# Performance work log

Measured on AMD Instinct MI355X. Metric: run time of the kernel, lower is better.

The kernel has to match this reference:

```python
import jax, jax.numpy as jnp
import numpy as np

B, N, F, FE, H, C = 2, 2048, 128, 8, 4, 64
LEAKY_ALPHA = 0.2
NEG_INF = -1e9


def setup_inputs() -> dict:
    key = jax.random.key(0)
    ks = jax.random.split(key, 8)
    return {
        "X": jax.random.normal(ks[0], (B, N, F), jnp.float32),
        "A": jax.random.uniform(ks[1], (B, N, N), jnp.float32),
        "E": jax.random.normal(ks[2], (B, N, N, FE), jnp.float32),
        "W_edge": jax.random.normal(ks[3], (FE, 1), jnp.float32) * 0.1,
        "b_edge": jnp.zeros((1,), jnp.float32),
        "W_gat": jax.random.normal(ks[4], (H, F, C), jnp.float32) * 0.05,
        "a_src": jax.random.normal(ks[5], (H, C), jnp.float32) * 0.1,
        "a_dst": jax.random.normal(ks[6], (H, C), jnp.float32) * 0.1,
        "b_gat": jnp.zeros((H * C,), jnp.float32),
        "ln_gamma": jnp.ones((H * C,), jnp.float32),
        "ln_beta": jnp.zeros((H * C,), jnp.float32),
    }


def reference(X, A, E, W_edge, b_edge, W_gat, a_src, a_dst, b_gat, ln_gamma, ln_beta):
    # --- edge gate: sigmoid(Dense_1(E)) -> [B,N,N], multiply into adjacency ---
    edge_w = jax.nn.sigmoid(jnp.einsum("bije,eo->bijo", E, W_edge) + b_edge)
    A = A * edge_w[..., 0]  # [B,N,N]

    # --- multi-head dense GAT (spektral GATConv, concat_heads, elu) ---
    h = jnp.einsum("bnf,hfc->bnhc", X, W_gat)  # [B,N,H,C]
    s_src = jnp.einsum("bnhc,hc->bnh", h, a_src)  # [B,N,H]
    s_dst = jnp.einsum("bnhc,hc->bnh", h, a_dst)
    # e_ij = LeakyReLU(src_i + dst_j): [B,N(i),N(j),H]
    logits = jax.nn.leaky_relu(s_src[:, :, None, :] + s_dst[:, None, :, :],
                               negative_slope=LEAKY_ALPHA)
    mask = jnp.where(A == 0.0, NEG_INF, 0.0)[..., None]  # [B,N,N,1]
    attn = jax.nn.softmax(logits + mask, axis=2)  # softmax over neighbors j
    out = jnp.einsum("bijh,bjhc->bihc", attn, h)  # [B,N,H,C]
    out = out.reshape(B, N, H * C) + b_gat
    out = jax.nn.elu(out)

    # --- LayerNorm over the feature axis (inference: dropout is identity) ---
    mu = jnp.mean(out, axis=-1, keepdims=True)
    var = jnp.var(out, axis=-1, keepdims=True)
    out = (out - mu) * jax.lax.rsqrt(var + 1e-3) * ln_gamma + ln_beta
    return out
```

## Files before the change

kernel.cpp:

```cpp
#include <hip/hip_runtime.h>
#include <hip/hip_bf16.h>


#define BB 2
#define NN 2048
#define FF 128
#define HH 4
#define CC 64
#define HC 256
#define TN 8
#define JB (NN / 8)
#define LOG2E 1.4426950408889634f

typedef __attribute__((ext_vector_type(8))) short short8;
typedef __attribute__((ext_vector_type(4))) float f32x4;

__device__ __forceinline__ float wave_sum(float v) {
#pragma unroll
    for (int m = 32; m >= 1; m >>= 1) v += __shfl_xor(v, m, 64);
    return v;
}

__device__ __forceinline__ unsigned short bf16rne(float x) {
    unsigned u = __float_as_uint(x);
    return (unsigned short)((u + 0x7fffu + ((u >> 16) & 1u)) >> 16);
}

__global__ __launch_bounds__(256) void k1_proj(
    const float* __restrict__ X, const float* __restrict__ Adj,
    const float* __restrict__ Wg,
    const float* __restrict__ a_src, const float* __restrict__ a_dst,
    unsigned short* __restrict__ hT, float* __restrict__ ssT,
    float* __restrict__ sdT, unsigned char* __restrict__ zT)
{
    const int blk = blockIdx.x;
    const int b  = blk / (NN / TN);
    const int n0 = (blk % (NN / TN)) * TN;
    const int tid = threadIdx.x;
    const int h = tid >> 6, c = tid & 63;

    float hv[TN];
#pragma unroll
    for (int r = 0; r < TN; ++r) hv[r] = 0.f;

    const float* xp = X + (size_t)(b * NN + n0) * FF;

#pragma unroll 4
    for (int f4 = 0; f4 < FF / 4; ++f4) {
        const int f = f4 * 4;
        const float w0 = Wg[(h * FF + f + 0) * CC + c];
        const float w1 = Wg[(h * FF + f + 1) * CC + c];
        const float w2 = Wg[(h * FF + f + 2) * CC + c];
        const float w3 = Wg[(h * FF + f + 3) * CC + c];
#pragma unroll
        for (int r = 0; r < TN; ++r) {
            float4 x4 = *(const float4*)(xp + r * FF + f);
            hv[r] = fmaf(x4.x, w0, hv[r]);
            hv[r] = fmaf(x4.y, w1, hv[r]);
            hv[r] = fmaf(x4.z, w2, hv[r]);
            hv[r] = fmaf(x4.w, w3, hv[r]);
        }
    }

    union { short8 v; unsigned short u[8]; } pk;
#pragma unroll
    for (int r = 0; r < TN; ++r) pk.u[r] = bf16rne(hv[r]);
    *(short8*)&hT[((((size_t)b * HH + h) * JB + (n0 >> 3)) * CC + c) * 8] = pk.v;

    const float as = a_src[tid];
    const float ad = a_dst[tid];
#pragma unroll
    for (int r = 0; r < TN; ++r) {
        const int n = n0 + r;
        float s1 = wave_sum(hv[r] * as);
        float s2 = wave_sum(hv[r] * ad);
        if (c == 0) {
            ssT[(b * HH + h) * NN + n] = s1 * LOG2E;
            sdT[(b * HH + h) * NN + n] = s2 * LOG2E;
        }
    }

    {
        const int r = tid >> 5;
        const int s = tid & 31;
        const size_t row = (size_t)(b * NN + n0 + r);
        const float* ap = Adj + row * NN + s * 64;
        unsigned char* zp = zT + (row << 8);
#pragma unroll
        for (int k = 0; k < 8; ++k) {
            float4 a0 = *(const float4*)(ap + k * 8);
            float4 a1 = *(const float4*)(ap + k * 8 + 4);
            unsigned m = 0u;
            m |= (a0.x == 0.f) ? 1u   : 0u;
            m |= (a0.y == 0.f) ? 2u   : 0u;
            m |= (a0.z == 0.f) ? 4u   : 0u;
            m |= (a0.w == 0.f) ? 8u   : 0u;
            m |= (a1.x == 0.f) ? 16u  : 0u;
            m |= (a1.y == 0.f) ? 32u  : 0u;
            m |= (a1.z == 0.f) ? 64u  : 0u;
            m |= (a1.w == 0.f) ? 128u : 0u;
            const int jb = s * 8 + k;
            const int jq = jb >> 6, rem = jb & 63;
            const int it = rem >> 2, lq = rem & 3;
            zp[jq * 64 + lq * 16 + it] = (unsigned char)m;
        }
    }
}

struct Stage {
    float4 sda, sdb;
    short8 bfr[4];
};

__device__ __forceinline__ void load_stage(
    Stage& s, const float* sdp, const unsigned short* hb, int it)
{
    const int js = it * 32;
    s.sda = *(const float4*)(sdp + js);
    s.sdb = *(const float4*)(sdp + js + 4);
    const unsigned short* hp = hb + it * 2048;
#pragma unroll
    for (int ni = 0; ni < 4; ++ni)
        s.bfr[ni] = *(const short8*)(hp + ni * 128);
}

__device__ __forceinline__ void consume_stage(
    const Stage& s, float ss, unsigned mb, float& lsum, f32x4* acc)
{
    const float sd[8] = {s.sda.x, s.sda.y, s.sda.z, s.sda.w,
                         s.sdb.x, s.sdb.y, s.sdb.z, s.sdb.w};
    float p[8];
#pragma unroll
    for (int t = 0; t < 8; ++t) {
        float x = ss + sd[t];
        x = fmaxf(x, 0.2f * x);
        float pv = __builtin_amdgcn_exp2f(x);
        p[t] = ((mb >> t) & 1u) ? 0.f : pv;
        lsum += p[t];
    }
    union { short8 v; __hip_bfloat162 h2[4]; } pk;
#pragma unroll
    for (int t = 0; t < 4; ++t)
        pk.h2[t] = __float22bfloat162_rn(make_float2(p[2 * t], p[2 * t + 1]));
#pragma unroll
    for (int ni = 0; ni < 4; ++ni)
        acc[ni] = __builtin_amdgcn_mfma_f32_16x16x32_bf16(pk.v, s.bfr[ni], acc[ni], 0, 0, 0);
}

__global__ __launch_bounds__(1024, 4) void k2_attn(
    const unsigned short* __restrict__ hT, const float* __restrict__ ssT,
    const float* __restrict__ sdT, const unsigned char* __restrict__ zT,
    const float* __restrict__ b_gat, const float* __restrict__ gamma,
    const float* __restrict__ beta, float* __restrict__ out)
{
    __shared__ float accs[3][16][HH][64];
    __shared__ float lsumx[3][HH][16];
    __shared__ float red1s[HH][16], red2s[HH][16];

    const int blk = blockIdx.x;
    const int b  = blk >> 7;
    const int i0 = (blk & 127) << 4;
    const int tid  = threadIdx.x;
    const int wave = tid >> 6;
    const int h  = wave & 3;
    const int jq = wave >> 2;
    const int l  = tid & 63;
    const int lr = l & 15;
    const int lq = l >> 4;

    const float ss = ssT[(b * HH + h) * NN + i0 + lr];

    const uint4 mw = *(const uint4*)(zT + ((size_t)(b * NN + i0 + lr) << 8)
                                       + jq * 64 + lq * 16);
    const unsigned long long mlo = ((unsigned long long)mw.y << 32) | mw.x;
    const unsigned long long mhi = ((unsigned long long)mw.w << 32) | mw.z;

    f32x4 acc[4];
#pragma unroll
    for (int ni = 0; ni < 4; ++ni) acc[ni] = (f32x4){0.f, 0.f, 0.f, 0.f};
    float lsum = 0.f;

    const float* sdp = sdT + (b * HH + h) * NN + jq * 512 + lq * 8;
    const unsigned short* hb =
        hT + ((((size_t)b * HH + h) * JB + jq * 64 + lq) * CC + lr) * 8;

    Stage s0, s1;
    load_stage(s0, sdp, hb, 0);
    load_stage(s1, sdp, hb, 1);
#pragma unroll 1
    for (int it = 0; it < 16; it += 2) {
        const unsigned long long msel = (it & 8) ? mhi : mlo;
        const int sh = (it & 7) * 8;
        const unsigned mb0 = (unsigned)(msel >> sh) & 0xffu;
        const unsigned mb1 = (unsigned)(msel >> (sh + 8)) & 0xffu;
        consume_stage(s0, ss, mb0, lsum, acc);
        if (it + 2 < 16) load_stage(s0, sdp, hb, it + 2);
        consume_stage(s1, ss, mb1, lsum, acc);
        if (it + 3 < 16) load_stage(s1, sdp, hb, it + 3);
    }

    lsum += __shfl_xor(lsum, 16, 64);
    lsum += __shfl_xor(lsum, 32, 64);

    if (jq > 0) {
        if (lq == 0) lsumx[jq - 1][h][lr] = lsum;
#pragma unroll
        for (int ni = 0; ni < 4; ++ni)
#pragma unroll
            for (int r = 0; r < 4; ++r)
                accs[jq - 1][ni * 4 + r][h][l] = acc[ni][r];
    }
    __syncthreads();

    if (jq == 0) {
        const float lcomb = lsum + lsumx[0][h][lr] + lsumx[1][h][lr] + lsumx[2][h][lr];
        float lrow[4];
#pragma unroll
        for (int r = 0; r < 4; ++r) lrow[r] = __shfl(lcomb, lq * 4 + r, 64);

        float bg[4];
#pragma unroll
        for (int ni = 0; ni < 4; ++ni) bg[ni] = b_gat[h * 64 + ni * 16 + lr];

        float vals[4][4];
        float s1[4] = {0.f, 0.f, 0.f, 0.f}, s2[4] = {0.f, 0.f, 0.f, 0.f};
#pragma unroll
        for (int ni = 0; ni < 4; ++ni)
#pragma unroll
            for (int r = 0; r < 4; ++r) {
                float a = acc[ni][r] + accs[0][ni * 4 + r][h][l]
                        + accs[1][ni * 4 + r][h][l] + accs[2][ni * 4 + r][h][l];
                float v = a / lrow[r] + bg[ni];
                v = (v > 0.f) ? v : (__expf(v) - 1.f);
                vals[ni][r] = v;
                s1[r] += v;
                s2[r] += v * v;
            }
#pragma unroll
        for (int m = 1; m <= 8; m <<= 1)
#pragma unroll
            for (int r = 0; r < 4; ++r) {
                s1[r] += __shfl_xor(s1[r], m, 64);
                s2[r] += __shfl_xor(s2[r], m, 64);
            }
        if (lr == 0)
#pragma unroll
            for (int r = 0; r < 4; ++r) {
                red1s[h][lq * 4 + r] = s1[r];
                red2s[h][lq * 4 + r] = s2[r];
            }
        __syncthreads();

        const float gm[4] = {gamma[h * 64 + lr], gamma[h * 64 + 16 + lr],
                             gamma[h * 64 + 32 + lr], gamma[h * 64 + 48 + lr]};
        const float bm[4] = {beta[h * 64 + lr], beta[h * 64 + 16 + lr],
                             beta[h * 64 + 32 + lr], beta[h * 64 + 48 + lr]};
#pragma unroll
        for (int r = 0; r < 4; ++r) {
            const int row = lq * 4 + r;
            float S1 = red1s[0][row] + red1s[1][row] + red1s[2][row] + red1s[3][row];
            float S2 = red2s[0][row] + red2s[1][row] + red2s[2][row] + red2s[3][row];
            float mu  = S1 * (1.f / HC);
            float var = S2 * (1.f / HC) - mu * mu;
            float inv = rsqrtf(var + 1e-3f);
            float* op = out + (size_t)(b * NN + i0 + row) * HC + h * 64 + lr;
#pragma unroll
            for (int ni = 0; ni < 4; ++ni)
                op[ni * 16] = (vals[ni][r] - mu) * inv * gm[ni] + bm[ni];
        }
    } else {
        __syncthreads();
    }
}

extern "C" void kernel_launch(void* const* d_in, const int* in_sizes, int n_in,
                              void* d_out, int out_size, void* d_ws, size_t ws_size,
                              hipStream_t stream)
{
    const float* X     = (const float*)d_in[0];
    const float* Adj   = (const float*)d_in[1];
    const float* Wg    = (const float*)d_in[5];
    const float* a_src = (const float*)d_in[6];
    const float* a_dst = (const float*)d_in[7];
    const float* b_gat = (const float*)d_in[8];
    const float* gam   = (const float*)d_in[9];
    const float* bet   = (const float*)d_in[10];
    float* out = (float*)d_out;

    const size_t hT_elems = (size_t)BB * HH * CC * NN;
    const size_t ss_elems = (size_t)BB * HH * NN;

    unsigned short* hT = (unsigned short*)d_ws;
    float* ssT = (float*)(hT + hT_elems);
    float* sdT = ssT + ss_elems;
    unsigned char* zT = (unsigned char*)(sdT + ss_elems);

    k1_proj<<<BB * NN / TN, 256, 0, stream>>>(X, Adj, Wg, a_src, a_dst, hT, ssT, sdT, zT);
    k2_attn<<<BB * (NN / 16), 1024, 0, stream>>>(hT, ssT, sdT, zT, b_gat, gam, bet, out);
}
```

Baseline: 369.9 us.

## Compute softmax denominators via MFMA, skip mask work when wave has none, vectorize LayerNorm

The row-sum of attention weights is now produced by an extra MFMA against a vector of bf16 ones instead of scalar adds and shuffles. Masking is applied only when some lane in the wave has a zero adjacency bit, so the per-element select is skipped in the common dense case. The LayerNorm epilogue is restructured so that all 16 waves each handle one row with float4 loads and stores, rather than only 4 waves doing strided scalar writes. The kernel also raises wave priority around the MFMA section. These changes add one MFMA per stage and an extra shared-memory round trip with an added barrier. The denominator is now summed from bf16-rounded weights, which matches the numerator's rounding.

```diff
diff --git a/kernel.cpp b/kernel.cpp
--- a/kernel.cpp
+++ b/kernel.cpp
@@ -125,26 +125,38 @@
 }
 
 __device__ __forceinline__ void consume_stage(
-    const Stage& s, float ss, unsigned mb, float& lsum, f32x4* acc)
+    const Stage& s, float ss, bool wz,
+    unsigned long long mlo, unsigned long long mhi, int it,
+    f32x4* acc, f32x4& accS, short8 onesv)
 {
     const float sd[8] = {s.sda.x, s.sda.y, s.sda.z, s.sda.w,
                          s.sdb.x, s.sdb.y, s.sdb.z, s.sdb.w};
     float p[8];
+    __builtin_amdgcn_s_setprio(1);
 #pragma unroll
     for (int t = 0; t < 8; ++t) {
         float x = ss + sd[t];
         x = fmaxf(x, 0.2f * x);
-        float pv = __builtin_amdgcn_exp2f(x);
-        p[t] = ((mb >> t) & 1u) ? 0.f : pv;
-        lsum += p[t];
+        p[t] = __builtin_amdgcn_exp2f(x);
+    }
+    if (wz) {
+        const unsigned mb =
+            (unsigned)(((it & 8) ? mhi : mlo) >> ((it & 7) * 8)) & 0xffu;
+        if (__any(mb != 0u)) {
+#pragma unroll
+            for (int t = 0; t < 8; ++t)
+                if ((mb >> t) & 1u) p[t] = 0.f;
+        }
     }
     union { short8 v; __hip_bfloat162 h2[4]; } pk;
 #pragma unroll
     for (int t = 0; t < 4; ++t)
         pk.h2[t] = __float22bfloat162_rn(make_float2(p[2 * t], p[2 * t + 1]));
+    accS = __builtin_amdgcn_mfma_f32_16x16x32_bf16(pk.v, onesv, accS, 0, 0, 0);
 #pragma unroll
     for (int ni = 0; ni < 4; ++ni)
         acc[ni] = __builtin_amdgcn_mfma_f32_16x16x32_bf16(pk.v, s.bfr[ni], acc[ni], 0, 0, 0);
+    __builtin_amdgcn_s_setprio(0);
 }
 
 __global__ __launch_bounds__(1024, 4) void k2_attn(
@@ -154,8 +166,7 @@
     const float* __restrict__ beta, float* __restrict__ out)
 {
     __shared__ float accs[3][16][HH][64];
-    __shared__ float lsumx[3][HH][16];
-    __shared__ float red1s[HH][16], red2s[HH][16];
+    __shared__ float lsumx[4][HH][16];
 
     const int blk = blockIdx.x;
     const int b  = blk >> 7;
@@ -174,11 +185,16 @@
                                        + jq * 64 + lq * 16);
     const unsigned long long mlo = ((unsigned long long)mw.y << 32) | mw.x;
     const unsigned long long mhi = ((unsigned long long)mw.w << 32) | mw.z;
+    const bool wz = __any((mlo | mhi) != 0ull);
+
+    short8 onesv;
+#pragma unroll
+    for (int i = 0; i < 8; ++i) onesv[i] = (short)0x3F80;
 
     f32x4 acc[4];
 #pragma unroll
     for (int ni = 0; ni < 4; ++ni) acc[ni] = (f32x4){0.f, 0.f, 0.f, 0.f};
-    float lsum = 0.f;
+    f32x4 accS = (f32x4){0.f, 0.f, 0.f, 0.f};
 
     const float* sdp = sdT + (b * HH + h) * NN + jq * 512 + lq * 8;
     const unsigned short* hb =
@@ -189,21 +205,17 @@
     load_stage(s1, sdp, hb, 1);
 #pragma unroll 1
     for (int it = 0; it < 16; it += 2) {
-        const unsigned long long msel = (it & 8) ? mhi : mlo;
-        const int sh = (it & 7) * 8;
-        const unsigned mb0 = (unsigned)(msel >> sh) & 0xffu;
-        const unsigned mb1 = (unsigned)(msel >> (sh + 8)) & 0xffu;
-        consume_stage(s0, ss, mb0, lsum, acc);
+        consume_stage(s0, ss, wz, mlo, mhi, it, acc, accS, onesv);
         if (it + 2 < 16) load_stage(s0, sdp, hb, it + 2);
-        consume_stage(s1, ss, mb1, lsum, acc);
+        consume_stage(s1, ss, wz, mlo, mhi, it + 1, acc, accS, onesv);
         if (it + 3 < 16) load_stage(s1, sdp, hb, it + 3);
     }
 
-    lsum += __shfl_xor(lsum, 16, 64);
-    lsum += __shfl_xor(lsum, 32, 64);
+    if (lr == 0)
+#pragma unroll
+        for (int r = 0; r < 4; ++r) lsumx[jq][h][lq * 4 + r] = accS[r];
 
     if (jq > 0) {
-        if (lq == 0) lsumx[jq - 1][h][lr] = lsum;
 #pragma unroll
         for (int ni = 0; ni < 4; ++ni)
 #pragma unroll
@@ -212,8 +224,10 @@
     }
     __syncthreads();
 
+    float vals[4][4];
     if (jq == 0) {
-        const float lcomb = lsum + lsumx[0][h][lr] + lsumx[1][h][lr] + lsumx[2][h][lr];
+        const float lcomb = lsumx[0][h][lr] + lsumx[1][h][lr]
+                          + lsumx[2][h][lr] + lsumx[3][h][lr];
         float lrow[4];
 #pragma unroll
         for (int r = 0; r < 4; ++r) lrow[r] = __shfl(lcomb, lq * 4 + r, 64);
@@ -222,8 +236,6 @@
 #pragma unroll
         for (int ni = 0; ni < 4; ++ni) bg[ni] = b_gat[h * 64 + ni * 16 + lr];
 
-        float vals[4][4];
-        float s1[4] = {0.f, 0.f, 0.f, 0.f}, s2[4] = {0.f, 0.f, 0.f, 0.f};
 #pragma unroll
         for (int ni = 0; ni < 4; ++ni)
 #pragma unroll
@@ -231,45 +243,42 @@
                 float a = acc[ni][r] + accs[0][ni * 4 + r][h][l]
                         + accs[1][ni * 4 + r][h][l] + accs[2][ni * 4 + r][h][l];
                 float v = a / lrow[r] + bg[ni];
-                v = (v > 0.f) ? v : (__expf(v) - 1.f);
-                vals[ni][r] = v;
-                s1[r] += v;
-                s2[r] += v * v;
+                vals[ni][r] = (v > 0.f) ? v : (__expf(v) - 1.f);
             }
-#pragma unroll
-        for (int m = 1; m <= 8; m <<= 1)
-#pragma unroll
-            for (int r = 0; r < 4; ++r) {
-                s1[r] += __shfl_xor(s1[r], m, 64);
-                s2[r] += __shfl_xor(s2[r], m, 64);
-            }
-        if (lr == 0)
-#pragma unroll
-            for (int r = 0; r < 4; ++r) {
-                red1s[h][lq * 4 + r] = s1[r];
-                red2s[h][lq * 4 + r] = s2[r];
-            }
-        __syncthreads();
-
-        const float gm[4] = {gamma[h * 64 + lr], gamma[h * 64 + 16 + lr],
-                             gamma[h * 64 + 32 + lr], gamma[h * 64 + 48 + lr]};
-        const float bm[4] = {beta[h * 64 + lr], beta[h * 64 + 16 + lr],
-                             beta[h * 64 + 32 + lr], beta[h * 64 + 48 + lr]};
-#pragma unroll
-        for (int r = 0; r < 4; ++r) {
-            const int row = lq * 4 + r;
-            float S1 = red1s[0][row] + red1s[1][row] + red1s[2][row] + red1s[3][row];
-            float S2 = red2s[0][row] + red2s[1][row] + red2s[2][row] + red2s[3][row];
-            float mu  = S1 * (1.f / HC);
-            float var = S2 * (1.f / HC) - mu * mu;
-            float inv = rsqrtf(var + 1e-3f);
-            float* op = out + (size_t)(b * NN + i0 + row) * HC + h * 64 + lr;
-#pragma unroll
-            for (int ni = 0; ni < 4; ++ni)
-                op[ni * 16] = (vals[ni][r] - mu) * inv * gm[ni] + bm[ni];
-        }
-    } else {
-        __syncthreads();
+    }
+    __syncthreads();
+
+    float* vbuf = &accs[0][0][0][0];
+    if (jq == 0) {
+#pragma unroll
+        for (int ni = 0; ni < 4; ++ni)
+#pragma unroll
+            for (int r = 0; r < 4; ++r)
+                vbuf[((h * 4 + ni) * 16 + (lq * 4 + r)) * 16 + lr] = vals[ni][r];
+    }
+    __syncthreads();
+
+    {
+        const int row = wave;
+        const int h2  = l >> 4;
+        const int ni2 = (l >> 2) & 3;
+        const int lr0 = (l & 3) * 4;
+        float4 v4 = *(const float4*)&vbuf[((h2 * 4 + ni2) * 16 + row) * 16 + lr0];
+
+        float S1 = wave_sum(v4.x + v4.y + v4.z + v4.w);
+        float S2 = wave_sum(v4.x * v4.x + v4.y * v4.y + v4.z * v4.z + v4.w * v4.w);
+        float mu  = S1 * (1.f / HC);
+        float var = S2 * (1.f / HC) - mu * mu;
+        float inv = rsqrtf(var + 1e-3f);
+
+        float4 gm = *(const float4*)&gamma[l * 4];
+        float4 bm = *(const float4*)&beta[l * 4];
+        float4 o;
+        o.x = (v4.x - mu) * inv * gm.x + bm.x;
+        o.y = (v4.y - mu) * inv * gm.y + bm.y;
+        o.z = (v4.z - mu) * inv * gm.z + bm.z;
+        o.w = (v4.w - mu) * inv * gm.w + bm.w;
+        *(float4*)(out + (size_t)(b * NN + i0 + row) * HC + l * 4) = o;
     }
 }
 
```

Result: no change. 370.4 us (+0.1%).
